# Optimization experiments

Measured on AMD Instinct MI355X. Metric: run time of the kernel, lower is better.

Reference implementation:

```python
import jax, jax.numpy as jnp
import numpy as np

V, H, O = 256, 1024, 1024   # input_dim, hidden_dim, output_dim
B, T = 64, 512


def setup_inputs() -> dict:
    key = jax.random.key(0)
    ks = jax.random.split(key, 12)
    s = 1.0 / np.sqrt(H)  # torch nn.RNN / nn.Linear init range
    u = lambda k, shp: jax.random.uniform(k, shp, jnp.float32, -s, s)
    return {
        "x": jax.random.randint(ks[0], (B, T), 0, V),
        "W_ih_f": u(ks[1], (H, V)), "W_hh_f": u(ks[2], (H, H)),
        "b_ih_f": u(ks[3], (H,)),   "b_hh_f": u(ks[4], (H,)),
        "W_ih_b": u(ks[5], (H, V)), "W_hh_b": u(ks[6], (H, H)),
        "b_ih_b": u(ks[7], (H,)),   "b_hh_b": u(ks[8], (H,)),
        "W_fc": u(ks[9], (O, 2 * H)), "b_fc": u(ks[10], (O,)),
    }


def _scan_rnn(xW, W_hh):
    # xW: [T,B,H] precomputed input contribution (x W_ih^T + b_ih + b_hh)
    def step(h, xw):
        h = jnp.tanh(xw + h @ W_hh.T)
        return h, h
    h0 = jnp.zeros((xW.shape[1], W_hh.shape[0]), xW.dtype)
    _, hs = jax.lax.scan(step, h0, xW)
    return hs  # [T,B,H]


def reference(x, W_ih_f, W_hh_f, b_ih_f, b_hh_f,
              W_ih_b, W_hh_b, b_ih_b, b_hh_b, W_fc, b_fc):
    # one_hot(x, V) @ W_ih^T  ==  W_ih.T[x]  (gather; same math, no dense one-hot)
    xW_f = W_ih_f.T[x] + b_ih_f + b_hh_f          # [B,T,H]
    xW_b = W_ih_b.T[x] + b_ih_b + b_hh_b          # [B,T,H]
    hf = _scan_rnn(jnp.swapaxes(xW_f, 0, 1), W_hh_f)            # [T,B,H]
    hb = _scan_rnn(jnp.swapaxes(xW_b, 0, 1)[::-1], W_hh_b)[::-1]  # [T,B,H]
    out = jnp.swapaxes(jnp.concatenate([hf, hb], axis=-1), 0, 1)  # [B,T,2H]
    return out @ W_fc.T + b_fc                    # [B,T,O]
```

## Files before the change

### kernel.cpp

```cpp
#include <hip/hip_runtime.h>
#include <math.h>

#define B_ 64
#define T_ 512
#define H_ 1024
#define V_ 256
#define O_ 1024
#define KFC 2048

typedef short bf16x8 __attribute__((ext_vector_type(8)));
typedef _Float16 f16x8 __attribute__((ext_vector_type(8)));
typedef float f32x4 __attribute__((ext_vector_type(4)));
typedef int   i32x4 __attribute__((ext_vector_type(4)));
typedef unsigned long long u64x2 __attribute__((ext_vector_type(2)));

#define FLIP64 0x8000800080008000ULL

#define OFF_TABLE_F 0
#define OFF_TABLE_B 1048576
#define OFF_XT      2097152
#define OFF_WHH     2228224
#define OFF_WFC     6422528
#define OFF_HSF     10616832
#define OFF_HSB     77725696

__device__ __forceinline__ float fast_tanh(float zz) {
  float e = __expf(2.0f * zz);
  return 1.0f - 2.0f * __builtin_amdgcn_rcpf(e + 1.0f);
}

__global__ void prep_kernel(const int* __restrict__ x,
    const float* __restrict__ WihF, const float* __restrict__ WhhF,
    const float* __restrict__ bihF, const float* __restrict__ bhhF,
    const float* __restrict__ WihB, const float* __restrict__ WhhB,
    const float* __restrict__ bihB, const float* __restrict__ bhhB,
    const float* __restrict__ Wfc,
    float* __restrict__ tableF, float* __restrict__ tableB,
    int* __restrict__ xT, short* __restrict__ whhpack,
    short* __restrict__ wfcpack, unsigned long long* __restrict__ hsz)
{
  const long NT1 = 524288, NT2 = 32768, NT3 = 2097152, NT4 = 2097152;
  const long NT5 = 16777216;
  const long total = NT1 + NT2 + NT3 + NT4 + NT5;
  for (long i = (long)blockIdx.x * blockDim.x + threadIdx.x; i < total;
       i += (long)gridDim.x * blockDim.x) {
    long j = i;
    if (j < NT1) {
      int d = (int)(j >> 18);
      int r = (int)(j & 262143);
      int v = r >> 10, h = r & 1023;
      const float* Wih = d ? WihB : WihF;
      const float* bi  = d ? bihB : bihF;
      const float* bh  = d ? bhhB : bhhF;
      (d ? tableB : tableF)[r] = Wih[h * V_ + v] + bi[h] + bh[h];
      continue;
    }
    j -= NT1;
    if (j < NT2) {
      int t = (int)(j >> 6), bb = (int)(j & 63);
      xT[j] = x[bb * T_ + t];
      continue;
    }
    j -= NT2;
    if (j < NT3) {
      int d = (int)(j >> 20);
      int r = (int)(j & 1048575);
      int jj = r & 7;
      int lanei = (r >> 3) & 63;
      int kt = (r >> 9) & 31;
      int cti = (r >> 14) & 3;
      int csi = (r >> 16) & 15;
      int c = csi * 64 + cti * 16 + (lanei & 15);
      int k = kt * 32 + (lanei >> 4) * 8 + jj;
      float w = (d ? WhhB : WhhF)[c * H_ + k];
      _Float16 wh = (_Float16)w;
      whhpack[j] = __builtin_bit_cast(short, wh);
      continue;
    }
    j -= NT3;
    if (j < NT4) {
      int jj = (int)(j & 7);
      int lanei = (int)((j >> 3) & 63);
      int nti = (int)((j >> 9) & 3);
      int k32 = (int)((j >> 11) & 63);
      int obi = (int)(j >> 17);
      int o = obi * 64 + nti * 16 + (lanei & 15);
      int k = k32 * 32 + (lanei >> 4) * 8 + jj;
      _Float16 wf = (_Float16)Wfc[(long)o * KFC + k];
      wfcpack[j] = __builtin_bit_cast(short, wf);
      continue;
    }
    j -= NT4;
    hsz[j] = 0ULL;
    continue;
  }
}

__global__ __launch_bounds__(256, 1)
void rnn_kernel(const int* __restrict__ xT,
                const float* __restrict__ tableF, const float* __restrict__ tableB,
                const short* __restrict__ whhpack,
                unsigned long long* __restrict__ hsfF,
                unsigned long long* __restrict__ hsfB)
{
  extern __shared__ char lds[];
  char* ldsW = lds;
  char* ldsH = lds + 131072;
  const int tid = threadIdx.x;
  const int wg = blockIdx.x;
  const int dir = wg >> 6;
  const int bt = (wg >> 4) & 3;
  const int cs = wg & 15;
  const int lane = tid & 63;
  const int ct = tid >> 6;
  const int row = bt * 16 + (lane & 15);
  const int c4 = cs * 64 + ct * 16 + (lane >> 4) * 4;
  const float* table = dir ? tableB : tableF;
  unsigned long long* hsx = dir ? hsfB : hsfF;
  const int pub_off = bt * 4096 + (c4 >> 5) * 128 + ((c4 >> 2) & 1) * 64 +
                      (lane & 15) + ((c4 >> 3) & 3) * 16;

  {
    const i32x4* wsrc = (const i32x4*)whhpack + (size_t)(dir * 16 + cs) * 8192;
    i32x4* wdst = (i32x4*)ldsW;
    #pragma unroll
    for (int it = 0; it < 32; ++it)
      wdst[it * 256 + tid] = wsrc[it * 256 + tid];
  }
  __syncthreads();

  const f32x4 zv = {0.f, 0.f, 0.f, 0.f};

  {
    int t0 = dir ? 511 : 0;
    int v = xT[t0 * 64 + row];
    f32x4 xwv = *(const f32x4*)(table + v * 1024 + c4);
    unsigned long long hx = 0;
    #pragma unroll
    for (int r = 0; r < 4; ++r) {
      float h = fast_tanh(xwv[r]);
      union { _Float16 f; unsigned short u; } cv; cv.f = (_Float16)h;
      unsigned short u = (cv.u == 0x8000u) ? 0u : cv.u;
      hx |= (unsigned long long)(u ^ 0x8000u) << (16 * r);
    }
    __hip_atomic_store(hsx + (size_t)t0 * 16384 + pub_off, hx,
                       __ATOMIC_RELAXED, __HIP_MEMORY_SCOPE_AGENT);
  }

#define LDX(p) __hip_atomic_load((p), __ATOMIC_RELAXED, __HIP_MEMORY_SCOPE_AGENT)

  for (int s = 1; s < 512; ++s) {
    const int t = dir ? (511 - s) : s;
    const int tprev = dir ? (t + 1) : (t - 1);
    int v = xT[t * 64 + row];
    f32x4 xwv = *(const f32x4*)(table + v * 1024 + c4);

    const unsigned long long* sp =
        hsx + (size_t)tprev * 16384 + bt * 4096 + tid * 2;
    unsigned long long a0[4], b0[4], a1[4], b1[4];
    #pragma unroll
    for (int i = 0; i < 4; ++i) {
      a0[i] = LDX(sp + i * 512);
      b0[i] = LDX(sp + i * 512 + 1);
    }
    #pragma unroll
    for (int i = 0; i < 4; ++i) {
      a1[i] = LDX(sp + (4 + i) * 512);
      b1[i] = LDX(sp + (4 + i) * 512 + 1);
    }

    for (;;) {
      int miss = 0;
      #pragma unroll
      for (int i = 0; i < 4; ++i)
        miss |= (a0[i] == 0ULL) | (b0[i] == 0ULL);
      if (!__ballot(miss)) break;
      __builtin_amdgcn_s_sleep(1);
      #pragma unroll
      for (int i = 0; i < 4; ++i) {
        a0[i] = LDX(sp + i * 512);
        b0[i] = LDX(sp + i * 512 + 1);
      }
    }
    #pragma unroll
    for (int jj = 0; jj < 4; ++jj) {
      u64x2 w; w[0] = a0[jj] ^ FLIP64; w[1] = b0[jj] ^ FLIP64;
      *(u64x2*)(ldsH + jj * 4096 + tid * 16) = w;
    }
    asm volatile("s_waitcnt lgkmcnt(0)" ::: "memory");
    __builtin_amdgcn_s_barrier();
    asm volatile("" ::: "memory");

    f32x4 acc4[4] = {zv, zv, zv, zv};
    #pragma unroll
    for (int kt = 0; kt < 16; ++kt) {
      f16x8 af = *(const f16x8*)(ldsW + ((ct * 32 + kt) * 64 + lane) * 16);
      u64x2 bv;
      bv[0] = *(const unsigned long long*)(ldsH + (kt * 128 + lane) * 8);
      bv[1] = *(const unsigned long long*)(ldsH + (kt * 128 + 64 + lane) * 8);
      f16x8 bf = __builtin_bit_cast(f16x8, bv);
      acc4[kt & 3] =
          __builtin_amdgcn_mfma_f32_16x16x32_f16(af, bf, acc4[kt & 3], 0, 0, 0);
    }

    for (;;) {
      int miss = 0;
      #pragma unroll
      for (int i = 0; i < 4; ++i)
        miss |= (a1[i] == 0ULL) | (b1[i] == 0ULL);
      if (!__ballot(miss)) break;
      __builtin_amdgcn_s_sleep(1);
      #pragma unroll
      for (int i = 0; i < 4; ++i) {
        a1[i] = LDX(sp + (4 + i) * 512);
        b1[i] = LDX(sp + (4 + i) * 512 + 1);
      }
    }
    #pragma unroll
    for (int jj = 0; jj < 4; ++jj) {
      u64x2 w; w[0] = a1[jj] ^ FLIP64; w[1] = b1[jj] ^ FLIP64;
      *(u64x2*)(ldsH + (4 + jj) * 4096 + tid * 16) = w;
    }
    asm volatile("s_waitcnt lgkmcnt(0)" ::: "memory");
    __builtin_amdgcn_s_barrier();
    asm volatile("" ::: "memory");

    #pragma unroll
    for (int kt = 16; kt < 32; ++kt) {
      f16x8 af = *(const f16x8*)(ldsW + ((ct * 32 + kt) * 64 + lane) * 16);
      u64x2 bv;
      bv[0] = *(const unsigned long long*)(ldsH + (kt * 128 + lane) * 8);
      bv[1] = *(const unsigned long long*)(ldsH + (kt * 128 + 64 + lane) * 8);
      f16x8 bf = __builtin_bit_cast(f16x8, bv);
      acc4[kt & 3] =
          __builtin_amdgcn_mfma_f32_16x16x32_f16(af, bf, acc4[kt & 3], 0, 0, 0);
    }

    f32x4 accs = (acc4[0] + acc4[1]) + (acc4[2] + acc4[3]);
    unsigned long long hx = 0;
    #pragma unroll
    for (int r = 0; r < 4; ++r) {
      float h = fast_tanh(accs[r] + xwv[r]);
      union { _Float16 f; unsigned short u; } cv; cv.f = (_Float16)h;
      unsigned short u = (cv.u == 0x8000u) ? 0u : cv.u;
      hx |= (unsigned long long)(u ^ 0x8000u) << (16 * r);
    }
    __hip_atomic_store(hsx + (size_t)t * 16384 + pub_off, hx,
                       __ATOMIC_RELAXED, __HIP_MEMORY_SCOPE_AGENT);
  }
#undef LDX
}

__global__ __launch_bounds__(256, 4)
void fc_kernel(const unsigned long long* __restrict__ hsfF,
               const unsigned long long* __restrict__ hsfB,
               const short* __restrict__ wfcpack, const float* __restrict__ bfc,
               float* __restrict__ out)
{
  __shared__ unsigned long long Alds[1024];
  __shared__ short Blds[4096];
  const int tid = threadIdx.x;
  const int lane = tid & 63;
  const int wv = tid >> 6;
  const int mt2 = wv & 1;
  const int nt2 = wv >> 1;
  const int t = blockIdx.x;
  const int ob = blockIdx.y;
  const int ik = tid >> 7;
  const int btl = (tid >> 5) & 3;
  const int w4 = (tid & 31) * 4;

  const i32x4 flip32 = {(int)0x80008000, (int)0x80008000,
                        (int)0x80008000, (int)0x80008000};
  f32x4 z = {0.f, 0.f, 0.f, 0.f};
  f32x4 acc[2][2] = {{z, z}, {z, z}};

  for (int kc = 0; kc < 32; ++kc) {
    {
      const unsigned long long* src =
          (kc < 16 ? hsfF : hsfB) + (size_t)t * 16384;
      int kt0 = (kc & 15) * 2;
      const unsigned long long* ap = src + btl * 4096 + (kt0 + ik) * 128 + w4;
      i32x4 a01 = *(const i32x4*)ap ^ flip32;
      i32x4 a23 = *(const i32x4*)(ap + 2) ^ flip32;
      *(i32x4*)&Alds[(btl * 2 + ik) * 128 + w4] = a01;
      *(i32x4*)&Alds[(btl * 2 + ik) * 128 + w4 + 2] = a23;
    }
    {
      const i32x4* src = (const i32x4*)(wfcpack + ((size_t)ob * 64 + kc * 2) * 2048);
      i32x4* dst = (i32x4*)Blds;
      dst[tid] = src[tid];
      dst[tid + 256] = src[tid + 256];
    }
    __syncthreads();
    #pragma unroll
    for (int k2 = 0; k2 < 2; ++k2) {
      f16x8 afr[2];
      #pragma unroll
      for (int mi = 0; mi < 2; ++mi) {
        int btm = mt2 * 2 + mi;
        u64x2 av;
        av[0] = Alds[(btm * 2 + k2) * 128 + lane];
        av[1] = Alds[(btm * 2 + k2) * 128 + 64 + lane];
        afr[mi] = __builtin_bit_cast(f16x8, av);
      }
      #pragma unroll
      for (int ni = 0; ni < 2; ++ni) {
        int ntg = nt2 * 2 + ni;
        f16x8 bfr = *(const f16x8*)((const char*)Blds + ((k2 * 4 + ntg) * 64 + lane) * 16);
        #pragma unroll
        for (int mi = 0; mi < 2; ++mi)
          acc[mi][ni] = __builtin_amdgcn_mfma_f32_16x16x32_f16(afr[mi], bfr, acc[mi][ni], 0, 0, 0);
      }
    }
    __syncthreads();
  }
  #pragma unroll
  for (int mi = 0; mi < 2; ++mi) {
    #pragma unroll
    for (int ni = 0; ni < 2; ++ni) {
      int o = ob * 64 + nt2 * 32 + ni * 16 + (lane & 15);
      float bias = bfc[o];
      #pragma unroll
      for (int r = 0; r < 4; ++r) {
        int b = mt2 * 32 + mi * 16 + (lane >> 4) * 4 + r;
        out[(size_t)(b * 512 + t) * O_ + o] = acc[mi][ni][r] + bias;
      }
    }
  }
}

extern "C" void kernel_launch(void* const* d_in, const int* in_sizes, int n_in,
                              void* d_out, int out_size, void* d_ws, size_t ws_size,
                              hipStream_t stream) {
  const int* x = (const int*)d_in[0];
  const float* WihF = (const float*)d_in[1];
  const float* WhhF = (const float*)d_in[2];
  const float* bihF = (const float*)d_in[3];
  const float* bhhF = (const float*)d_in[4];
  const float* WihB = (const float*)d_in[5];
  const float* WhhB = (const float*)d_in[6];
  const float* bihB = (const float*)d_in[7];
  const float* bhhB = (const float*)d_in[8];
  const float* Wfc  = (const float*)d_in[9];
  const float* bfc  = (const float*)d_in[10];
  float* out = (float*)d_out;
  char* ws = (char*)d_ws;

  float* tableF = (float*)(ws + OFF_TABLE_F);
  float* tableB = (float*)(ws + OFF_TABLE_B);
  int* xT = (int*)(ws + OFF_XT);
  short* whhpack = (short*)(ws + OFF_WHH);
  short* wfcpack = (short*)(ws + OFF_WFC);
  unsigned long long* hsfF = (unsigned long long*)(ws + OFF_HSF);
  unsigned long long* hsfB = (unsigned long long*)(ws + OFF_HSB);

  hipFuncSetAttribute((const void*)rnn_kernel,
                      hipFuncAttributeMaxDynamicSharedMemorySize, 163840);

  prep_kernel<<<dim3(2048), dim3(256), 0, stream>>>(
      x, WihF, WhhF, bihF, bhhF, WihB, WhhB, bihB, bhhB, Wfc,
      tableF, tableB, xT, whhpack, wfcpack, hsfF);
  rnn_kernel<<<dim3(128), dim3(256), 163840, stream>>>(
      xT, tableF, tableB, whhpack, hsfF, hsfB);
  fc_kernel<<<dim3(512, 16), dim3(256), 0, stream>>>(
      hsfF, hsfB, wfcpack, bfc, out);
}
```

Before: 1.642 ms.

## Keep recurrent weights in registers and widen FC tiles per wave

The RNN kernel now loads each wave's W_hh slice into 32 f16x8 registers once, instead of staging it in LDS and re-reading it every timestep. This removes per-step LDS traffic for the weight operand and shrinks dynamic LDS from 160KB to 32KB, at the cost of about 128 extra VGPRs per thread. The FC kernel is restructured so each wave handles its own timestep with a 4x4 MFMA tile, so a block covers 4 timesteps and the W_fc tile staged in LDS is reused across them. This raises register pressure in the FC kernel, and its launch bound drops to 2 blocks per SM.

```diff
diff --git a/kernel.cpp b/kernel.cpp
--- a/kernel.cpp
+++ b/kernel.cpp
@@ -104,8 +104,7 @@
                 unsigned long long* __restrict__ hsfB)
 {
   extern __shared__ char lds[];
-  char* ldsW = lds;
-  char* ldsH = lds + 131072;
+  char* ldsH = lds;
   const int tid = threadIdx.x;
   const int wg = blockIdx.x;
   const int dir = wg >> 6;
@@ -120,14 +119,13 @@
   const int pub_off = bt * 4096 + (c4 >> 5) * 128 + ((c4 >> 2) & 1) * 64 +
                       (lane & 15) + ((c4 >> 3) & 3) * 16;
 
+  f16x8 Wreg[32];
   {
     const i32x4* wsrc = (const i32x4*)whhpack + (size_t)(dir * 16 + cs) * 8192;
-    i32x4* wdst = (i32x4*)ldsW;
-    #pragma unroll
-    for (int it = 0; it < 32; ++it)
-      wdst[it * 256 + tid] = wsrc[it * 256 + tid];
-  }
-  __syncthreads();
+    #pragma unroll
+    for (int kt = 0; kt < 32; ++kt)
+      Wreg[kt] = __builtin_bit_cast(f16x8, wsrc[(ct * 32 + kt) * 64 + lane]);
+  }
 
   const f32x4 zv = {0.f, 0.f, 0.f, 0.f};
 
@@ -194,13 +192,12 @@
     f32x4 acc4[4] = {zv, zv, zv, zv};
     #pragma unroll
     for (int kt = 0; kt < 16; ++kt) {
-      f16x8 af = *(const f16x8*)(ldsW + ((ct * 32 + kt) * 64 + lane) * 16);
       u64x2 bv;
       bv[0] = *(const unsigned long long*)(ldsH + (kt * 128 + lane) * 8);
       bv[1] = *(const unsigned long long*)(ldsH + (kt * 128 + 64 + lane) * 8);
       f16x8 bf = __builtin_bit_cast(f16x8, bv);
       acc4[kt & 3] =
-          __builtin_amdgcn_mfma_f32_16x16x32_f16(af, bf, acc4[kt & 3], 0, 0, 0);
+          __builtin_amdgcn_mfma_f32_16x16x32_f16(Wreg[kt], bf, acc4[kt & 3], 0, 0, 0);
     }
 
     for (;;) {
@@ -227,13 +224,12 @@
 
     #pragma unroll
     for (int kt = 16; kt < 32; ++kt) {
-      f16x8 af = *(const f16x8*)(ldsW + ((ct * 32 + kt) * 64 + lane) * 16);
       u64x2 bv;
       bv[0] = *(const unsigned long long*)(ldsH + (kt * 128 + lane) * 8);
       bv[1] = *(const unsigned long long*)(ldsH + (kt * 128 + 64 + lane) * 8);
       f16x8 bf = __builtin_bit_cast(f16x8, bv);
       acc4[kt & 3] =
-          __builtin_amdgcn_mfma_f32_16x16x32_f16(af, bf, acc4[kt & 3], 0, 0, 0);
+          __builtin_amdgcn_mfma_f32_16x16x32_f16(Wreg[kt], bf, acc4[kt & 3], 0, 0, 0);
     }
 
     f32x4 accs = (acc4[0] + acc4[1]) + (acc4[2] + acc4[3]);
@@ -251,40 +247,46 @@
 #undef LDX
 }
 
-__global__ __launch_bounds__(256, 4)
+__global__ __launch_bounds__(256, 2)
 void fc_kernel(const unsigned long long* __restrict__ hsfF,
                const unsigned long long* __restrict__ hsfB,
                const short* __restrict__ wfcpack, const float* __restrict__ bfc,
                float* __restrict__ out)
 {
-  __shared__ unsigned long long Alds[1024];
+  __shared__ unsigned long long Alds[4096];
   __shared__ short Blds[4096];
   const int tid = threadIdx.x;
   const int lane = tid & 63;
-  const int wv = tid >> 6;
-  const int mt2 = wv & 1;
-  const int nt2 = wv >> 1;
-  const int t = blockIdx.x;
+  const int w = tid >> 6;
+  const int t = blockIdx.x * 4 + w;
   const int ob = blockIdx.y;
-  const int ik = tid >> 7;
-  const int btl = (tid >> 5) & 3;
-  const int w4 = (tid & 31) * 4;
+  const int btl = lane >> 4;
+  const int li = lane & 15;
 
   const i32x4 flip32 = {(int)0x80008000, (int)0x80008000,
                         (int)0x80008000, (int)0x80008000};
   f32x4 z = {0.f, 0.f, 0.f, 0.f};
-  f32x4 acc[2][2] = {{z, z}, {z, z}};
+  f32x4 acc[4][4] = {{z, z, z, z}, {z, z, z, z}, {z, z, z, z}, {z, z, z, z}};
+  unsigned long long* Aw = &Alds[w * 1024];
 
   for (int kc = 0; kc < 32; ++kc) {
     {
       const unsigned long long* src =
           (kc < 16 ? hsfF : hsfB) + (size_t)t * 16384;
       int kt0 = (kc & 15) * 2;
-      const unsigned long long* ap = src + btl * 4096 + (kt0 + ik) * 128 + w4;
-      i32x4 a01 = *(const i32x4*)ap ^ flip32;
-      i32x4 a23 = *(const i32x4*)(ap + 2) ^ flip32;
-      *(i32x4*)&Alds[(btl * 2 + ik) * 128 + w4] = a01;
-      *(i32x4*)&Alds[(btl * 2 + ik) * 128 + w4 + 2] = a23;
+      const unsigned long long* ap = src + btl * 4096 + kt0 * 128 + li * 8;
+      #pragma unroll
+      for (int rr = 0; rr < 2; ++rr) {
+        i32x4 q0 = *(const i32x4*)(ap + rr * 128) ^ flip32;
+        i32x4 q1 = *(const i32x4*)(ap + rr * 128 + 2) ^ flip32;
+        i32x4 q2 = *(const i32x4*)(ap + rr * 128 + 4) ^ flip32;
+        i32x4 q3 = *(const i32x4*)(ap + rr * 128 + 6) ^ flip32;
+        unsigned long long* dst = &Aw[(btl * 2 + rr) * 128 + li * 8];
+        *(i32x4*)(dst) = q0;
+        *(i32x4*)(dst + 2) = q1;
+        *(i32x4*)(dst + 4) = q2;
+        *(i32x4*)(dst + 6) = q3;
+      }
     }
     {
       const i32x4* src = (const i32x4*)(wfcpack + ((size_t)ob * 64 + kc * 2) * 2048);
@@ -295,35 +297,33 @@
     __syncthreads();
     #pragma unroll
     for (int k2 = 0; k2 < 2; ++k2) {
-      f16x8 afr[2];
-      #pragma unroll
-      for (int mi = 0; mi < 2; ++mi) {
-        int btm = mt2 * 2 + mi;
+      f16x8 afr[4];
+      #pragma unroll
+      for (int mi = 0; mi < 4; ++mi) {
         u64x2 av;
-        av[0] = Alds[(btm * 2 + k2) * 128 + lane];
-        av[1] = Alds[(btm * 2 + k2) * 128 + 64 + lane];
+        av[0] = Aw[(mi * 2 + k2) * 128 + lane];
+        av[1] = Aw[(mi * 2 + k2) * 128 + 64 + lane];
         afr[mi] = __builtin_bit_cast(f16x8, av);
       }
       #pragma unroll
-      for (int ni = 0; ni < 2; ++ni) {
-        int ntg = nt2 * 2 + ni;
-        f16x8 bfr = *(const f16x8*)((const char*)Blds + ((k2 * 4 + ntg) * 64 + lane) * 16);
+      for (int ni = 0; ni < 4; ++ni) {
+        f16x8 bfr = *(const f16x8*)((const char*)Blds + ((k2 * 4 + ni) * 64 + lane) * 16);
         #pragma unroll
-        for (int mi = 0; mi < 2; ++mi)
+        for (int mi = 0; mi < 4; ++mi)
           acc[mi][ni] = __builtin_amdgcn_mfma_f32_16x16x32_f16(afr[mi], bfr, acc[mi][ni], 0, 0, 0);
       }
     }
     __syncthreads();
   }
   #pragma unroll
-  for (int mi = 0; mi < 2; ++mi) {
-    #pragma unroll
-    for (int ni = 0; ni < 2; ++ni) {
-      int o = ob * 64 + nt2 * 32 + ni * 16 + (lane & 15);
+  for (int mi = 0; mi < 4; ++mi) {
+    #pragma unroll
+    for (int ni = 0; ni < 4; ++ni) {
+      int o = ob * 64 + ni * 16 + (lane & 15);
       float bias = bfc[o];
       #pragma unroll
       for (int r = 0; r < 4; ++r) {
-        int b = mt2 * 32 + mi * 16 + (lane >> 4) * 4 + r;
+        int b = mi * 16 + (lane >> 4) * 4 + r;
         out[(size_t)(b * 512 + t) * O_ + o] = acc[mi][ni][r] + bias;
       }
     }
@@ -356,13 +356,13 @@
   unsigned long long* hsfB = (unsigned long long*)(ws + OFF_HSB);
 
   hipFuncSetAttribute((const void*)rnn_kernel,
-                      hipFuncAttributeMaxDynamicSharedMemorySize, 163840);
+                      hipFuncAttributeMaxDynamicSharedMemorySize, 32768);
 
   prep_kernel<<<dim3(2048), dim3(256), 0, stream>>>(
       x, WihF, WhhF, bihF, bhhF, WihB, WhhB, bihB, bhhB, Wfc,
       tableF, tableB, xT, whhpack, wfcpack, hsfF);
-  rnn_kernel<<<dim3(128), dim3(256), 163840, stream>>>(
+  rnn_kernel<<<dim3(128), dim3(256), 32768, stream>>>(
       xT, tableF, tableB, whhpack, hsfF, hsfB);
-  fc_kernel<<<dim3(512, 16), dim3(256), 0, stream>>>(
+  fc_kernel<<<dim3(128, 16), dim3(256), 0, stream>>>(
       hsfF, hsfB, wfcpack, bfc, out);
 }
```

Result: faster. 1.553 ms (-5.4%).
